# Optimization experiments

Hardware: AMD Instinct MI355X
Metric: run time of the kernel (lower is better)

## Reference

```python
import jax, jax.numpy as jnp
import numpy as np

B, C, H, W = 128, 8, 144, 144
TW, OG = 5, 2          # token_window, off_grid
NCLS, DT = 6, 256      # num_cls, dim_token
ITC = C * H * TW       # in_token_channel = 5760
EPS = 1e-5


def setup_inputs() -> dict:
    key = jax.random.key(0)
    ks = jax.random.split(key, 40)
    n = jax.random.normal
    u = jax.random.uniform
    CW = C * W  # 1152
    inp = {
        'x': n(ks[0], (B, C, H, W), jnp.float32),
        # ext head: Conv1d(1152,256,1) -> BN(256) -> Conv1d(256,2,1)
        'ext_w1': n(ks[1], (256, CW)) * 0.02, 'ext_b1': jnp.zeros((256,)),
        'ext_g': jnp.ones((256,)), 'ext_bb': jnp.zeros((256,)),
        'ext_m': n(ks[2], (256,)) * 0.1, 'ext_v': u(ks[3], (256,), minval=0.5, maxval=1.5),
        'ext_w2': n(ks[4], (2, 256)) * 0.05, 'ext_b2': jnp.zeros((2,)),
        # cls head: Conv1d(1152,256,1) -> BN(256) -> Conv1d(256,144,1)
        'cls_w1': n(ks[5], (256, CW)) * 0.02, 'cls_b1': jnp.zeros((256,)),
        'cls_g': jnp.ones((256,)), 'cls_bb': jnp.zeros((256,)),
        'cls_m': n(ks[6], (256,)) * 0.1, 'cls_v': u(ks[7], (256,), minval=0.5, maxval=1.5),
        'cls_w2': n(ks[8], (W, 256)) * 0.05, 'cls_b2': jnp.zeros((W,)),
        # to_token Linear(5760,256) and class embeddings
        'tok_w': n(ks[9], (ITC, DT)) * 0.01, 'tok_b': jnp.zeros((DT,)),
        'emb': n(ks[10], (NCLS, DT)),
        # transformer (depth=1, heads=2, dim_head=32 -> inner=64)
        'ln1_g': jnp.ones((DT,)), 'ln1_b': jnp.zeros((DT,)),
        'qkv_w': n(ks[11], (DT, 3 * 64)) * 0.05,
        'out_w': n(ks[12], (64, DT)) * 0.05, 'out_b': jnp.zeros((DT,)),
        'ln2_g': jnp.ones((DT,)), 'ln2_b': jnp.zeros((DT,)),
        'ff_w1': n(ks[13], (DT, 512)) * 0.05, 'ff_b1': jnp.zeros((512,)),
        'ff_w2': n(ks[14], (512, DT)) * 0.05, 'ff_b2': jnp.zeros((DT,)),
        'lnf_g': jnp.ones((DT,)), 'lnf_b': jnp.zeros((DT,)),
        'fin_w': n(ks[15], (DT, ITC)) * 0.02, 'fin_b': jnp.zeros((ITC,)),
    }
    return inp


def _ln(z, g, b):
    mu = jnp.mean(z, -1, keepdims=True)
    var = jnp.var(z, -1, keepdims=True)
    return (z - mu) * jax.lax.rsqrt(var + EPS) * g + b


def reference(x, ext_w1, ext_b1, ext_g, ext_bb, ext_m, ext_v, ext_w2, ext_b2,
              cls_w1, cls_b1, cls_g, cls_bb, cls_m, cls_v, cls_w2, cls_b2,
              tok_w, tok_b, emb,
              ln1_g, ln1_b, qkv_w, out_w, out_b,
              ln2_g, ln2_b, ff_w1, ff_b1, ff_w2, ff_b2,
              lnf_g, lnf_b, fin_w, fin_b):

    def head(row, w1, b1, g, bet, m, v, w2, b2):
        # row: [B, C*W, H]; 1x1 conv = per-position GEMM, BN in eval mode
        h = jnp.einsum('oc,bch->boh', w1, row) + b1[:, None]
        h = (h - m[:, None]) * jax.lax.rsqrt(v[:, None] + EPS) * g[:, None] + bet[:, None]
        h = jnp.einsum('oc,bch->boh', w2, h) + b2[:, None]
        return jnp.transpose(h, (0, 2, 1))  # [B, H, out]

    def heads_on(xx):
        # 'b c h w -> b (c w) h' (c major, w minor)
        row = jnp.transpose(xx, (0, 1, 3, 2)).reshape(B, C * W, H)
        e = jax.nn.softmax(head(row, ext_w1, ext_b1, ext_g, ext_bb, ext_m, ext_v, ext_w2, ext_b2), axis=2)
        c = jax.nn.softmax(head(row, cls_w1, cls_b1, cls_g, cls_bb, cls_m, cls_v, cls_w2, cls_b2), axis=2)
        return e, c

    ext, cls = heads_on(x)
    xp = jnp.pad(x, ((0, 0), (0, 0), (0, 0), (OG, OG)))  # [B,C,H,W+4]

    argmax_col = jnp.argmax(cls, axis=2)                  # [B,H]
    idx = argmax_col[:, :, None] + jnp.arange(TW)         # window in padded coords

    def transformer(t):  # t: [B, N, DT]
        z = _ln(t, ln1_g, ln1_b)
        q, k, v = jnp.split(z @ qkv_w, 3, axis=-1)
        sp = lambda a: a.reshape(B, -1, 2, 32).transpose(0, 2, 1, 3)  # b h n d
        q, k, v = sp(q), sp(k), sp(v)
        att = jax.nn.softmax(jnp.einsum('bhnd,bhmd->bhnm', q, k) * (32 ** -0.5), axis=-1)
        o = jnp.einsum('bhnm,bhmd->bhnd', att, v).transpose(0, 2, 1, 3).reshape(B, -1, 64)
        t = o @ out_w + out_b + t
        z = _ln(t, ln2_g, ln2_b)
        t = jax.nn.gelu(z @ ff_w1 + ff_b1, approximate=False) @ ff_w2 + ff_b2 + t
        t = _ln(t, lnf_g, lnf_b)
        return (t @ fin_w + fin_b).reshape(B, -1, C, H, TW)  # [B,N,C,H,TW]

    def refine(xpad):
        g_idx = jnp.broadcast_to(idx[:, None], (B, C, H, TW))
        patches = jnp.take_along_axis(xpad, g_idx, axis=3)    # [B,C,H,TW]
        tok = patches.reshape(B, -1) @ tok_w + tok_b          # [B,DT]
        tokens = tok[:, None, :] + emb[None]                  # [B,NCLS,DT]
        refined = transformer(tokens)                         # [B,NCLS,C,H,TW]
        xpt = jnp.transpose(xpad, (0, 2, 3, 1))               # [B,H,Wp,C]
        bb = jnp.arange(B)[:, None, None]
        hh = jnp.arange(H)[None, :, None]
        for i in range(NCLS):
            xpt = xpt.at[bb, hh, idx].set(jnp.transpose(refined[:, i], (0, 2, 3, 1)))
        return jnp.transpose(xpt, (0, 3, 1, 2))

    xp = jax.lax.cond(jnp.mean(ext[:, :, 0]) > 0.3, refine, lambda a: a, xp)
    x2 = xp[:, :, :, OG:W + OG]
    ext2, cls2 = heads_on(x2)
    return ext, cls, ext2, cls2
```

## Files before the change

kernel.cpp:

```cpp
#include <hip/hip_runtime.h>
#include <math.h>

#define EPSF 1e-5f
#define GAPTH 1e-3f
#define NKS 4
#define KSL 288
#define RROWS 18432


typedef __attribute__((ext_vector_type(8))) short short8v;
typedef __attribute__((ext_vector_type(4))) float f32x4;
typedef unsigned short ushort;
typedef unsigned int uint;

__device__ inline ushort f2bf(float f) {
    uint u = __float_as_uint(f);
    uint r = (u + 0x7FFFu + ((u >> 16) & 1u)) >> 16;
    return (ushort)r;
}
__device__ inline float bf2f(ushort h) { return __uint_as_float(((uint)h) << 16); }

__global__ __launch_bounds__(256) void wcomb_build(
    const float* __restrict__ w1e, const float* __restrict__ b1e, const float* __restrict__ ge,
    const float* __restrict__ bbe, const float* __restrict__ me, const float* __restrict__ ve,
    const float* __restrict__ w2e, const float* __restrict__ b2e,
    const float* __restrict__ w1c, const float* __restrict__ b1c, const float* __restrict__ gc,
    const float* __restrict__ bbc, const float* __restrict__ mc, const float* __restrict__ vc,
    const float* __restrict__ w2c, const float* __restrict__ b2c,
    float* __restrict__ Wc32, ushort* __restrict__ Wchi, ushort* __restrict__ Wclo,
    float* __restrict__ cconst)
{
    __shared__ float coef[256];
    __shared__ float csum[4];
    const int j = blockIdx.x, kq = blockIdx.y, tid = threadIdx.x;
    const int lane = tid & 63, wid = tid >> 6;

    const float *w1 = nullptr, *w2row = nullptr, *b1 = nullptr, *g = nullptr,
                *bb = nullptr, *m = nullptr, *v = nullptr;
    float b2v = 0.f;
    int valid = 0;
    if (j < 144) {
        valid = 1; w1 = w1c; w2row = w2c + (size_t)j * 256;
        b1 = b1c; g = gc; bb = bbc; m = mc; v = vc; b2v = b2c[j];
    } else if (j < 146) {
        valid = 1; w1 = w1e; w2row = w2e + (size_t)(j - 144) * 256;
        b1 = b1e; g = ge; bb = bbe; m = me; v = ve; b2v = b2e[j - 144];
    }

    float cf = 0.f, cc = 0.f;
    if (valid) {
        float s = g[tid] * rsqrtf(v[tid] + EPSF);
        float w2v = w2row[tid];
        cf = w2v * s;
        cc = w2v * ((b1[tid] - m[tid]) * s + bb[tid]);
    }
    coef[tid] = cf;
    if (kq == 0) {
        float t = cc;
#pragma unroll
        for (int off = 32; off; off >>= 1) t += __shfl_xor(t, off);
        if (lane == 0) csum[wid] = t;
    }
    __syncthreads();
    if (kq == 0 && tid == 0)
        cconst[j] = valid ? ((csum[0] + csum[1]) + (csum[2] + csum[3]) + b2v) : 0.f;

    for (int k = kq * KSL + tid; k < (kq + 1) * KSL; k += 256) {
        float acc = 0.f;
        if (valid) {
            for (int o = 0; o < 256; o++) acc += coef[o] * w1[(size_t)o * 1152 + k];
        }
        Wc32[(size_t)j * 1152 + k] = acc;
        ushort hi = f2bf(acc);
        Wchi[(size_t)j * 1152 + k] = hi;
        Wclo[(size_t)j * 1152 + k] = f2bf(acc - bf2f(hi));
    }
}

__global__ void zero_counters(int* __restrict__ cand_count)
{
    *cand_count = 0;
}

__global__ __launch_bounds__(256) void transpose_w(
    const float* __restrict__ src, float* __restrict__ dst, int R, int Cc)
{
    __shared__ float tile[32][33];
    const int rb = blockIdx.y * 32, cb = blockIdx.x * 32;
    const int tx = threadIdx.x & 31, ty = threadIdx.x >> 5;
#pragma unroll
    for (int i = ty; i < 32; i += 8) {
        int r = rb + i, c = cb + tx;
        tile[i][tx] = (r < R && c < Cc) ? src[(size_t)r * Cc + c] : 0.f;
    }
    __syncthreads();
#pragma unroll
    for (int i = ty; i < 32; i += 8) {
        int c = cb + i, r = rb + tx;
        if (c < Cc && r < R) dst[(size_t)c * R + r] = tile[tx][i];
    }
}

__global__ __launch_bounds__(256) void logits_gemm(
    const float* __restrict__ x, const ushort* __restrict__ Wchi, const ushort* __restrict__ Wclo,
    float* __restrict__ logits_part)
{
    __shared__ ushort Ahi[128][40], Alo[128][40], Bhi[160][40], Blo[160][40];
    const int tid = threadIdx.x;
    const int lane = tid & 63, wid = tid >> 6;
    const int wm = wid & 1, wn = wid >> 1;
    const int rb = blockIdx.x * 128;
    const int ks = blockIdx.y;
    const int kbase = ks * KSL;
    const int NIT = KSL / 32;

    const int rl = tid >> 1, kq = (tid & 1) << 4;
    const int arow = rb + rl;
    const int ab = arow / 144, ahh = arow - ab * 144;
    const int br2 = 128 + (tid >> 1);

    float av[16];
    short8v vb0a, vb0b, vl0a, vl0b;
    short8v vb2a, vb2b, vl2a, vl2b;

    auto LOAD = [&](int kb) {
        const int k0 = kb + kq;
        const int c = k0 / 144, w = k0 - c * 144;
        const float* xp = x + (((size_t)(ab * 8 + c) * 144 + ahh) * 144 + w);
#pragma unroll
        for (int q = 0; q < 4; q++) {
            const float4 t4 = *reinterpret_cast<const float4*>(xp + q * 4);
            av[q * 4 + 0] = t4.x; av[q * 4 + 1] = t4.y;
            av[q * 4 + 2] = t4.z; av[q * 4 + 3] = t4.w;
        }
        const ushort* bh = Wchi + (size_t)rl * 1152 + k0;
        const ushort* bl = Wclo + (size_t)rl * 1152 + k0;
        vb0a = *reinterpret_cast<const short8v*>(bh);
        vb0b = *reinterpret_cast<const short8v*>(bh + 8);
        vl0a = *reinterpret_cast<const short8v*>(bl);
        vl0b = *reinterpret_cast<const short8v*>(bl + 8);
        if (tid < 64) {
            const ushort* bh2 = Wchi + (size_t)br2 * 1152 + k0;
            const ushort* bl2 = Wclo + (size_t)br2 * 1152 + k0;
            vb2a = *reinterpret_cast<const short8v*>(bh2);
            vb2b = *reinterpret_cast<const short8v*>(bh2 + 8);
            vl2a = *reinterpret_cast<const short8v*>(bl2);
            vl2b = *reinterpret_cast<const short8v*>(bl2 + 8);
        }
    };

    auto STORE = [&]() {
        short8v hv0, hv1, lv0, lv1;
#pragma unroll
        for (int q = 0; q < 8; q++) {
            ushort h = f2bf(av[q]);
            hv0[q] = (short)h; lv0[q] = (short)f2bf(av[q] - bf2f(h));
        }
#pragma unroll
        for (int q = 0; q < 8; q++) {
            ushort h = f2bf(av[8 + q]);
            hv1[q] = (short)h; lv1[q] = (short)f2bf(av[8 + q] - bf2f(h));
        }
        *reinterpret_cast<short8v*>(&Ahi[rl][kq]) = hv0;
        *reinterpret_cast<short8v*>(&Ahi[rl][kq + 8]) = hv1;
        *reinterpret_cast<short8v*>(&Alo[rl][kq]) = lv0;
        *reinterpret_cast<short8v*>(&Alo[rl][kq + 8]) = lv1;
        *reinterpret_cast<short8v*>(&Bhi[rl][kq]) = vb0a;
        *reinterpret_cast<short8v*>(&Bhi[rl][kq + 8]) = vb0b;
        *reinterpret_cast<short8v*>(&Blo[rl][kq]) = vl0a;
        *reinterpret_cast<short8v*>(&Blo[rl][kq + 8]) = vl0b;
        if (tid < 64) {
            *reinterpret_cast<short8v*>(&Bhi[br2][kq]) = vb2a;
            *reinterpret_cast<short8v*>(&Bhi[br2][kq + 8]) = vb2b;
            *reinterpret_cast<short8v*>(&Blo[br2][kq]) = vl2a;
            *reinterpret_cast<short8v*>(&Blo[br2][kq + 8]) = vl2b;
        }
    };

    f32x4 acc[4][5];
#pragma unroll
    for (int mt = 0; mt < 4; mt++)
#pragma unroll
        for (int nt = 0; nt < 5; nt++) acc[mt][nt] = (f32x4){0.f, 0.f, 0.f, 0.f};

    const int fr = lane & 15, fg = (lane >> 4) << 3;

    LOAD(kbase);
    for (int t = 0; t < NIT; t++) {
        STORE();
        if (t < NIT - 1) LOAD(kbase + (t + 1) * 32);
        __syncthreads();
        short8v ah[4], al[4];
#pragma unroll
        for (int mt = 0; mt < 4; mt++) {
            ah[mt] = *reinterpret_cast<const short8v*>(&Ahi[wm * 64 + mt * 16 + fr][fg]);
            al[mt] = *reinterpret_cast<const short8v*>(&Alo[wm * 64 + mt * 16 + fr][fg]);
        }
#pragma unroll
        for (int nt = 0; nt < 5; nt++) {
            short8v bh = *reinterpret_cast<const short8v*>(&Bhi[wn * 80 + nt * 16 + fr][fg]);
            short8v bl = *reinterpret_cast<const short8v*>(&Blo[wn * 80 + nt * 16 + fr][fg]);
#pragma unroll
            for (int mt = 0; mt < 4; mt++) {
                acc[mt][nt] = __builtin_amdgcn_mfma_f32_16x16x32_bf16(ah[mt], bh, acc[mt][nt], 0, 0, 0);
                acc[mt][nt] = __builtin_amdgcn_mfma_f32_16x16x32_bf16(ah[mt], bl, acc[mt][nt], 0, 0, 0);
                acc[mt][nt] = __builtin_amdgcn_mfma_f32_16x16x32_bf16(al[mt], bh, acc[mt][nt], 0, 0, 0);
            }
        }
        __syncthreads();
    }

    float* base = logits_part + (size_t)ks * RROWS * 160;
#pragma unroll
    for (int mt = 0; mt < 4; mt++) {
#pragma unroll
        for (int nt = 0; nt < 5; nt++) {
            int gcol = wn * 80 + nt * 16 + fr;
            if (gcol < 146) {
                float* dst = base + (size_t)(rb + wm * 64 + mt * 16 + ((lane >> 4) << 2)) * 160 + gcol;
#pragma unroll
                for (int i = 0; i < 4; i++)
                    dst[(size_t)i * 160] = acc[mt][nt][i];
            }
        }
    }
}

template<int DELTA>
__global__ __launch_bounds__(256) void softmax_heads(
    const float* __restrict__ logits_part, const float* __restrict__ cconst,
    float* __restrict__ out_cls, float* __restrict__ out_ext,
    int* __restrict__ amax, float* __restrict__ partials,
    int* __restrict__ cand_count, int* __restrict__ cand_list,
    const float* __restrict__ x, const float* __restrict__ WcT,
    const float* __restrict__ refined5, const int* __restrict__ flag)
{
    __shared__ float ps[4];
    __shared__ float dL[4][148];
    __shared__ float dsh[4][40];
    __shared__ int   ksh[4][40];
    const int r4 = threadIdx.x >> 6, lane = threadIdx.x & 63;
    const int row = blockIdx.x * 4 + r4;

    if (DELTA) {
        const int fl = *flag;
        if (fl) {
            const int b = row / 144, hh = row - b * 144;
            const int a = amax[row];
            if (lane < 40) {
                int c = lane / 5, tw = lane - c * 5;
                int w = a - 2 + tw;
                float d = 0.f; int k = 0;
                if (w >= 0 && w < 144) {
                    k = c * 144 + w;
                    d = refined5[(size_t)b * 5760 + (c * 144 + hh) * 5 + tw]
                      - x[((size_t)(b * 8 + c) * 144 + hh) * 144 + w];
                }
                dsh[r4][lane] = d; ksh[r4][lane] = k;
            }
            __syncthreads();
#pragma unroll
            for (int rj = 0; rj < 3; rj++) {
                int j = lane + rj * 64;
                if (j < 146) {
                    float acc = 0.f;
#pragma unroll 8
                    for (int i = 0; i < 40; i++)
                        acc += WcT[(size_t)ksh[r4][i] * 160 + j] * dsh[r4][i];
                    dL[r4][j] = acc;
                }
            }
        } else {
#pragma unroll
            for (int rj = 0; rj < 3; rj++) {
                int j = lane + rj * 64;
                if (j < 146) dL[r4][j] = 0.f;
            }
        }
        __syncthreads();
    }

    const float* L0 = logits_part + (size_t)row * 160;
    const float* L1 = L0 + (size_t)RROWS * 160;
    const float* L2 = L1 + (size_t)RROWS * 160;
    const float* L3 = L2 + (size_t)RROWS * 160;
    float v0 = L0[lane] + L1[lane] + L2[lane] + L3[lane] + cconst[lane];
    float v1 = L0[lane + 64] + L1[lane + 64] + L2[lane + 64] + L3[lane + 64] + cconst[lane + 64];
    float v2 = (lane < 16) ? (L0[lane + 128] + L1[lane + 128] + L2[lane + 128] + L3[lane + 128]
                              + cconst[lane + 128])
                           : -3.0e38f;
    if (DELTA) {
        v0 += dL[r4][lane];
        v1 += dL[r4][lane + 64];
        if (lane < 16) v2 += dL[r4][lane + 128];
    }
    float m = v0; int mi = lane;
    if (v1 > m) { m = v1; mi = lane + 64; }
    if (v2 > m) { m = v2; mi = lane + 128; }
    float m1 = v0, m2 = -3.0e38f;
    if (v1 > m1) { m2 = m1; m1 = v1; } else m2 = v1;
    if (v2 > m1) { m2 = m1; m1 = v2; } else m2 = fmaxf(m2, v2);
#pragma unroll
    for (int off = 32; off; off >>= 1) {
        float om = __shfl_xor(m, off);
        int   oi = __shfl_xor(mi, off);
        if (om > m || (om == m && oi < mi)) { m = om; mi = oi; }
        float om1 = __shfl_xor(m1, off);
        float om2 = __shfl_xor(m2, off);
        float nm1 = fmaxf(m1, om1);
        m2 = fmaxf(fminf(m1, om1), fmaxf(m2, om2));
        m1 = nm1;
    }
    float e0 = expf(v0 - m), e1 = expf(v1 - m);
    float e2 = (lane < 16) ? expf(v2 - m) : 0.f;
    float s = e0 + e1 + e2;
#pragma unroll
    for (int off = 32; off; off >>= 1) s += __shfl_xor(s, off);
    float inv = 1.f / s;
    float* O = out_cls + (size_t)row * 144;
    O[lane] = e0 * inv;
    O[lane + 64] = e1 * inv;
    if (lane < 16) O[lane + 128] = e2 * inv;

    float l0 = L0[144] + L1[144] + L2[144] + L3[144] + cconst[144];
    float l1 = L0[145] + L1[145] + L2[145] + L3[145] + cconst[145];
    if (DELTA) { l0 += dL[r4][144]; l1 += dL[r4][145]; }
    float mx = fmaxf(l0, l1);
    float ee0 = expf(l0 - mx), ee1 = expf(l1 - mx);
    float einv = 1.f / (ee0 + ee1);
    float p0 = ee0 * einv;
    if (lane == 0) {
        out_ext[(size_t)row * 2] = p0;
        out_ext[(size_t)row * 2 + 1] = ee1 * einv;
        if (amax != nullptr && !DELTA) {
            amax[row] = mi;
            if (m1 - m2 < GAPTH) {
                int slot = atomicAdd(cand_count, 1);
                cand_list[slot] = row;
            }
        }
    }
    if (partials != nullptr) {
        if (lane == 0) ps[r4] = p0;
        __syncthreads();
        if (threadIdx.x == 0) partials[blockIdx.x] = (ps[0] + ps[1]) + (ps[2] + ps[3]);
    }
}

__global__ __launch_bounds__(256) void reduce_flag(const float* __restrict__ partials, int n,
                                                   int* __restrict__ flag)
{
    __shared__ float sm[256];
    int tid = threadIdx.x;
    float s = 0.f;
    for (int i = tid; i < n; i += 256) s += partials[i];
    sm[tid] = s; __syncthreads();
    for (int off = 128; off; off >>= 1) {
        if (tid < off) sm[tid] += sm[tid + off];
        __syncthreads();
    }
    if (tid == 0) *flag = (sm[0] * (1.f / 18432.f) > 0.3f) ? 1 : 0;
}

__global__ __launch_bounds__(256) void fixup_list(
    const int* __restrict__ cand_count, const int* __restrict__ cand_list,
    const float* __restrict__ x,
    const float* __restrict__ w1cT, const float* __restrict__ b1c,
    const float* __restrict__ gc, const float* __restrict__ bbc,
    const float* __restrict__ mc, const float* __restrict__ vc,
    const float* __restrict__ w2cT, const float* __restrict__ b2c,
    int* __restrict__ amax)
{
    __shared__ float xrow[1152];
    __shared__ float hsh[256];
    __shared__ float Lsh[144];
    const int tid = threadIdx.x;
    const int n = *cand_count;

    for (int ci = blockIdx.x; ci < n; ci += gridDim.x) {
        const int row = cand_list[ci];
        const int b = row / 144, hh = row - b * 144;
        for (int e = tid; e < 1152; e += 256) {
            int c = e / 144, w = e - c * 144;
            xrow[e] = x[(((size_t)(b * 8 + c) * 144 + hh) * 144) + w];
        }
        __syncthreads();
        {
            float a = 0.f;
#pragma unroll 8
            for (int k = 0; k < 1152; k++) a += w1cT[(size_t)k * 256 + tid] * xrow[k];
            float sc = gc[tid] * rsqrtf(vc[tid] + EPSF);
            hsh[tid] = (a + b1c[tid] - mc[tid]) * sc + bbc[tid];
        }
        __syncthreads();
        if (tid < 144) {
            float a = 0.f;
#pragma unroll 8
            for (int k = 0; k < 256; k++) a += w2cT[(size_t)k * 144 + tid] * hsh[k];
            Lsh[tid] = a + b2c[tid];
        }
        __syncthreads();
        if (tid == 0) {
            int bi = 0; float bv = Lsh[0];
            for (int j = 1; j < 144; j++) if (Lsh[j] > bv) { bv = Lsh[j]; bi = j; }
            amax[row] = bi;
        }
        __syncthreads();
    }
}

__global__ __launch_bounds__(256) void tok_partial(const float* __restrict__ x,
    const int* __restrict__ amax, const float* __restrict__ tok_w, float* __restrict__ tpart)
{
    __shared__ float P[720];
    __shared__ int ash[144];
    int b = blockIdx.x, c = blockIdx.y, tid = threadIdx.x;
    if (tid < 144) ash[tid] = amax[b * 144 + tid];
    __syncthreads();
    for (int e = tid; e < 720; e += 256) {
        int hh = e / 5, tw = e - hh * 5;
        int w = ash[hh] + tw - 2;
        P[e] = (w >= 0 && w < 144) ? x[(((size_t)(b * 8 + c) * 144 + hh) * 144) + w] : 0.f;
    }
    __syncthreads();
    const float* wbase = tok_w + (size_t)c * 720 * 256;
    float a0 = 0.f, a1 = 0.f, a2 = 0.f, a3 = 0.f;
    for (int k = 0; k < 720; k += 4) {
        a0 += P[k]     * wbase[(size_t)k * 256 + tid];
        a1 += P[k + 1] * wbase[(size_t)(k + 1) * 256 + tid];
        a2 += P[k + 2] * wbase[(size_t)(k + 2) * 256 + tid];
        a3 += P[k + 3] * wbase[(size_t)(k + 3) * 256 + tid];
    }
    tpart[((size_t)b * 8 + c) * 256 + tid] = (a0 + a1) + (a2 + a3);
}

__global__ __launch_bounds__(512) void attn_front(
    const float* __restrict__ tpart, const float* __restrict__ tok_b,
    const float* __restrict__ emb,
    const float* __restrict__ ln1_g, const float* __restrict__ ln1_b,
    const float* __restrict__ qkv_w,
    const float* __restrict__ out_w, const float* __restrict__ out_b,
    const float* __restrict__ ln2_g, const float* __restrict__ ln2_b,
    float* __restrict__ z2_5, float* __restrict__ t5out)
{
    __shared__ float s[256];
    __shared__ float z[6][256];
    __shared__ float qk[6][192];
    __shared__ float att[2][6];
    __shared__ float o5[64];
    __shared__ float t5[256];
    __shared__ float stat[2];
    const int b = blockIdx.x, tid = threadIdx.x;
    const int lane = tid & 63, wv = tid >> 6;
    const int g4 = tid >> 2, l4 = tid & 3;

    if (tid < 256) {
        float a = tok_b[tid];
#pragma unroll
        for (int ks = 0; ks < 8; ks++) a += tpart[((size_t)b * 8 + ks) * 256 + tid];
        s[tid] = a;
    }
    __syncthreads();

    if (wv < 6) {
        float y[4], s1 = 0.f, s2 = 0.f;
#pragma unroll
        for (int q = 0; q < 4; q++) {
            int k = lane + 64 * q;
            y[q] = s[k] + emb[wv * 256 + k];
            s1 += y[q]; s2 += y[q] * y[q];
        }
#pragma unroll
        for (int off = 32; off; off >>= 1) { s1 += __shfl_xor(s1, off); s2 += __shfl_xor(s2, off); }
        float mu = s1 * (1.f / 256.f);
        float var = s2 * (1.f / 256.f) - mu * mu;
        float rs = rsqrtf(var + EPSF);
#pragma unroll
        for (int q = 0; q < 4; q++) {
            int k = lane + 64 * q;
            z[wv][k] = (y[q] - mu) * rs * ln1_g[k] + ln1_b[k];
        }
    }
    __syncthreads();

    for (int tt = g4; tt < 832; tt += 128) {
        int i, c;
        if (tt < 768) { i = tt >> 7; c = 64 + (tt & 127); }
        else          { i = 5;       c = tt - 768; }
        float a = 0.f;
#pragma unroll 8
        for (int j = 0; j < 64; j++) {
            int k = l4 + 4 * j;
            a += z[i][k] * qkv_w[(size_t)k * 192 + c];
        }
        a += __shfl_xor(a, 1);
        a += __shfl_xor(a, 2);
        if (l4 == 0) qk[i][c] = a;
    }
    __syncthreads();

    if (tid < 12) {
        int h = tid / 6, j = tid - h * 6;
        float a = 0.f;
#pragma unroll
        for (int d = 0; d < 32; d++) a += qk[5][h * 32 + d] * qk[j][64 + h * 32 + d];
        att[h][j] = a * 0.17677669529663687f;
    }
    __syncthreads();
    if (tid < 2) {
        float m = -3.0e38f;
        for (int j = 0; j < 6; j++) m = fmaxf(m, att[tid][j]);
        float ssum = 0.f;
        for (int j = 0; j < 6; j++) { float e = expf(att[tid][j] - m); att[tid][j] = e; ssum += e; }
        float inv = 1.f / ssum;
        for (int j = 0; j < 6; j++) att[tid][j] *= inv;
    }
    __syncthreads();
    if (tid < 64) {
        int h = tid >> 5;
        float a = 0.f;
#pragma unroll
        for (int j = 0; j < 6; j++) a += att[h][j] * qk[j][128 + tid];
        o5[tid] = a;
    }
    __syncthreads();

    for (int tt = g4; tt < 256; tt += 128) {
        float a = 0.f;
#pragma unroll
        for (int j = 0; j < 16; j++) {
            int d = l4 + 4 * j;
            a += o5[d] * out_w[(size_t)d * 256 + tt];
        }
        a += __shfl_xor(a, 1);
        a += __shfl_xor(a, 2);
        if (l4 == 0) t5[tt] = a + out_b[tt] + s[tt] + emb[5 * 256 + tt];
    }
    __syncthreads();

    if (wv == 0) {
        float s1 = 0.f, s2 = 0.f;
#pragma unroll
        for (int q = 0; q < 4; q++) { float vv = t5[lane + 64 * q]; s1 += vv; s2 += vv * vv; }
#pragma unroll
        for (int off = 32; off; off >>= 1) { s1 += __shfl_xor(s1, off); s2 += __shfl_xor(s2, off); }
        if (lane == 0) {
            float mu = s1 * (1.f / 256.f);
            float var = s2 * (1.f / 256.f) - mu * mu;
            stat[0] = mu; stat[1] = rsqrtf(var + EPSF);
        }
    }
    __syncthreads();
    if (tid < 256) {
        t5out[(size_t)b * 256 + tid] = t5[tid];
        z2_5[(size_t)b * 256 + tid] = (t5[tid] - stat[0]) * stat[1] * ln2_g[tid] + ln2_b[tid];
    }
}

__global__ __launch_bounds__(512) void ff1_gelu(
    const float* __restrict__ z2_5, const float* __restrict__ ff_w1,
    const float* __restrict__ ff_b1, float* __restrict__ f5)
{
    __shared__ float zsh[256];
    const int b = blockIdx.x, half = blockIdx.y, tid = threadIdx.x;
    const int g4 = tid >> 2, l4 = tid & 3;
    if (tid < 256) zsh[tid] = z2_5[(size_t)b * 256 + tid];
    __syncthreads();
    for (int tt = g4; tt < 256; tt += 128) {
        const int jj = half * 256 + tt;
        float a = 0.f;
#pragma unroll 8
        for (int j = 0; j < 64; j++) {
            int k = l4 + 4 * j;
            a += zsh[k] * ff_w1[(size_t)k * 512 + jj];
        }
        a += __shfl_xor(a, 1);
        a += __shfl_xor(a, 2);
        if (l4 == 0) {
            a += ff_b1[jj];
            f5[(size_t)b * 512 + jj] = 0.5f * a * (1.f + erff(a * 0.70710678118654752f));
        }
    }
}

__global__ __launch_bounds__(512) void ff2_lnf(
    const float* __restrict__ f5, const float* __restrict__ ff_w2,
    const float* __restrict__ ff_b2, const float* __restrict__ t5in,
    const float* __restrict__ lnf_g, const float* __restrict__ lnf_b,
    float* __restrict__ tfin)
{
    __shared__ float fsh[512];
    __shared__ float tsh[256];
    __shared__ float stat[2];
    const int b = blockIdx.x, tid = threadIdx.x;
    const int lane = tid & 63, wv = tid >> 6;
    const int g4 = tid >> 2, l4 = tid & 3;
    fsh[tid] = f5[(size_t)b * 512 + tid];
    __syncthreads();
    for (int tt = g4; tt < 256; tt += 128) {
        float a = 0.f;
#pragma unroll 8
        for (int j = 0; j < 128; j++) {
            int k = l4 + 4 * j;
            a += fsh[k] * ff_w2[(size_t)k * 256 + tt];
        }
        a += __shfl_xor(a, 1);
        a += __shfl_xor(a, 2);
        if (l4 == 0) tsh[tt] = a + ff_b2[tt] + t5in[(size_t)b * 256 + tt];
    }
    __syncthreads();
    if (wv == 0) {
        float s1 = 0.f, s2 = 0.f;
#pragma unroll
        for (int q = 0; q < 4; q++) { float vv = tsh[lane + 64 * q]; s1 += vv; s2 += vv * vv; }
#pragma unroll
        for (int off = 32; off; off >>= 1) { s1 += __shfl_xor(s1, off); s2 += __shfl_xor(s2, off); }
        if (lane == 0) {
            float mu = s1 * (1.f / 256.f);
            float var = s2 * (1.f / 256.f) - mu * mu;
            stat[0] = mu; stat[1] = rsqrtf(var + EPSF);
        }
    }
    __syncthreads();
    if (tid < 256)
        tfin[(size_t)b * 256 + tid] = (tsh[tid] - stat[0]) * stat[1] * lnf_g[tid] + lnf_b[tid];
}

__global__ __launch_bounds__(256) void fin_gemm(const float* __restrict__ tfin,
    const float* __restrict__ fin_w, const float* __restrict__ fin_b, float* __restrict__ refined5)
{
    __shared__ float tf[16][256];
    int tid = threadIdx.x;
    int nb = blockIdx.x * 256 + tid;
    int bg = blockIdx.y * 16;
    for (int e = tid; e < 4096; e += 256) tf[e >> 8][e & 255] = tfin[(size_t)(bg + (e >> 8)) * 256 + (e & 255)];
    __syncthreads();
    if (nb < 5760) {
        float acc[16];
#pragma unroll
        for (int bb = 0; bb < 16; bb++) acc[bb] = 0.f;
        for (int k = 0; k < 256; k++) {
            float wv = fin_w[(size_t)k * 5760 + nb];
#pragma unroll
            for (int bb = 0; bb < 16; bb++) acc[bb] += tf[bb][k] * wv;
        }
        float fb = fin_b[nb];
#pragma unroll
        for (int bb = 0; bb < 16; bb++)
            refined5[(size_t)(bg + bb) * 5760 + nb] = acc[bb] + fb;
    }
}

extern "C" void kernel_launch(void* const* d_in, const int* in_sizes, int n_in,
                              void* d_out, int out_size, void* d_ws, size_t ws_size,
                              hipStream_t stream)
{
    const float* x      = (const float*)d_in[0];
    const float* ext_w1 = (const float*)d_in[1];
    const float* ext_b1 = (const float*)d_in[2];
    const float* ext_g  = (const float*)d_in[3];
    const float* ext_bb = (const float*)d_in[4];
    const float* ext_m  = (const float*)d_in[5];
    const float* ext_v  = (const float*)d_in[6];
    const float* ext_w2 = (const float*)d_in[7];
    const float* ext_b2 = (const float*)d_in[8];
    const float* cls_w1 = (const float*)d_in[9];
    const float* cls_b1 = (const float*)d_in[10];
    const float* cls_g  = (const float*)d_in[11];
    const float* cls_bb = (const float*)d_in[12];
    const float* cls_m  = (const float*)d_in[13];
    const float* cls_v  = (const float*)d_in[14];
    const float* cls_w2 = (const float*)d_in[15];
    const float* cls_b2 = (const float*)d_in[16];
    const float* tok_w  = (const float*)d_in[17];
    const float* tok_b  = (const float*)d_in[18];
    const float* emb    = (const float*)d_in[19];
    const float* ln1_g  = (const float*)d_in[20];
    const float* ln1_b  = (const float*)d_in[21];
    const float* qkv_w  = (const float*)d_in[22];
    const float* out_w  = (const float*)d_in[23];
    const float* out_b  = (const float*)d_in[24];
    const float* ln2_g  = (const float*)d_in[25];
    const float* ln2_b  = (const float*)d_in[26];
    const float* ff_w1  = (const float*)d_in[27];
    const float* ff_b1  = (const float*)d_in[28];
    const float* ff_w2  = (const float*)d_in[29];
    const float* ff_b2  = (const float*)d_in[30];
    const float* lnf_g  = (const float*)d_in[31];
    const float* lnf_b  = (const float*)d_in[32];
    const float* fin_w  = (const float*)d_in[33];
    const float* fin_b  = (const float*)d_in[34];

    float* out = (float*)d_out;
    float* ws  = (float*)d_ws;

    float*  Wc32     = ws;
    float*  cconst   = ws + 184320;
    ushort* Wchi     = (ushort*)(ws + 184480);
    ushort* Wclo     = (ushort*)(ws + 276640);
    float*  logitsP  = ws + 368800;
    float*  partials = ws + 12165280;
    float*  z2_5     = ws + 12169888;
    float*  t5buf    = ws + 12202656;
    float*  f5buf    = ws + 12235424;
    float*  tfin     = ws + 12300960;
    float*  refined5 = ws + 12333728;
    float*  tpart    = ws + 13071008;
    int*    amax     = (int*)(ws + 13333152);
    int*    flag     = (int*)(ws + 13351584);
    int*    cand_cnt = (int*)(ws + 13351585);
    int*    cand_lst = (int*)(ws + 13351586);
    float*  w1cT     = ws + 13370020;
    float*  w2cT     = ws + 13664932;
    float*  WcT      = ws + 13701796;

    float* out_ext  = out;
    float* out_cls  = out + 36864;
    float* out_ext2 = out + 2691072;
    float* out_cls2 = out + 2727936;

    dim3 blk(256);

    wcomb_build<<<dim3(160, 4), blk, 0, stream>>>(
        ext_w1, ext_b1, ext_g, ext_bb, ext_m, ext_v, ext_w2, ext_b2,
        cls_w1, cls_b1, cls_g, cls_bb, cls_m, cls_v, cls_w2, cls_b2,
        Wc32, Wchi, Wclo, cconst);
    zero_counters<<<1, 1, 0, stream>>>(cand_cnt);
    transpose_w<<<dim3(36, 8), blk, 0, stream>>>(cls_w1, w1cT, 256, 1152);
    transpose_w<<<dim3(8, 5), blk, 0, stream>>>(cls_w2, w2cT, 144, 256);
    transpose_w<<<dim3(36, 5), blk, 0, stream>>>(Wc32, WcT, 160, 1152);

    logits_gemm<<<dim3(144, NKS), blk, 0, stream>>>(x, Wchi, Wclo, logitsP);
    softmax_heads<0><<<4608, blk, 0, stream>>>(logitsP, cconst, out_cls, out_ext, amax, partials,
        cand_cnt, cand_lst, nullptr, nullptr, nullptr, nullptr);
    reduce_flag<<<1, blk, 0, stream>>>(partials, 4608, flag);
    fixup_list<<<256, blk, 0, stream>>>(cand_cnt, cand_lst, x,
        w1cT, cls_b1, cls_g, cls_bb, cls_m, cls_v, w2cT, cls_b2, amax);

    tok_partial<<<dim3(128, 8), blk, 0, stream>>>(x, amax, tok_w, tpart);
    attn_front<<<128, dim3(512), 0, stream>>>(tpart, tok_b, emb, ln1_g, ln1_b, qkv_w,
        out_w, out_b, ln2_g, ln2_b, z2_5, t5buf);
    ff1_gelu<<<dim3(128, 2), dim3(512), 0, stream>>>(z2_5, ff_w1, ff_b1, f5buf);
    ff2_lnf<<<128, dim3(512), 0, stream>>>(f5buf, ff_w2, ff_b2, t5buf, lnf_g, lnf_b, tfin);
    fin_gemm<<<dim3(23, 8), blk, 0, stream>>>(tfin, fin_w, fin_b, refined5);

    softmax_heads<1><<<4608, blk, 0, stream>>>(logitsP, cconst, out_cls2, out_ext2, amax, nullptr,
        nullptr, nullptr, x, WcT, refined5, flag);
}
```

Measured before the change: 307.8 us.

## Halve logits GEMM M-tile, halve split-K, and lower ambiguity threshold

The logits GEMM now uses 64-row tiles with 2 K-splits instead of 128-row tiles with 4, so the grid doubles in M while the partial-logit buffer and the softmax reduction shrink from four partials to two. Workspace offsets are repacked to match. The fixup kernel's dot products are split into four independent accumulators to add ILP. GAPTH is lowered, so fewer rows count as argmax candidates needing exact fp32 recompute. That saves fixup work but relies on the bf16 hi/lo split GEMM being precise enough near ties.

New measurement: 278.3 us. 9.6% less time.

```diff
diff --git a/kernel.cpp b/kernel.cpp
--- a/kernel.cpp
+++ b/kernel.cpp
@@ -2,9 +2,9 @@
 #include <math.h>
 
 #define EPSF 1e-5f
-#define GAPTH 1e-3f
-#define NKS 4
-#define KSL 288
+#define GAPTH 2e-4f
+#define NKS 2
+#define KSL 576
 #define RROWS 18432
 
 
@@ -65,7 +65,7 @@
     if (kq == 0 && tid == 0)
         cconst[j] = valid ? ((csum[0] + csum[1]) + (csum[2] + csum[3]) + b2v) : 0.f;
 
-    for (int k = kq * KSL + tid; k < (kq + 1) * KSL; k += 256) {
+    for (int k = kq * 288 + tid; k < (kq + 1) * 288; k += 256) {
         float acc = 0.f;
         if (valid) {
             for (int o = 0; o < 256; o++) acc += coef[o] * w1[(size_t)o * 1152 + k];
@@ -105,81 +105,69 @@
     const float* __restrict__ x, const ushort* __restrict__ Wchi, const ushort* __restrict__ Wclo,
     float* __restrict__ logits_part)
 {
-    __shared__ ushort Ahi[128][40], Alo[128][40], Bhi[160][40], Blo[160][40];
+    __shared__ ushort Ahi[64][40], Alo[64][40], Bhi[160][40], Blo[160][40];
     const int tid = threadIdx.x;
     const int lane = tid & 63, wid = tid >> 6;
     const int wm = wid & 1, wn = wid >> 1;
-    const int rb = blockIdx.x * 128;
+    const int rb = blockIdx.x * 64;
     const int ks = blockIdx.y;
     const int kbase = ks * KSL;
     const int NIT = KSL / 32;
 
-    const int rl = tid >> 1, kq = (tid & 1) << 4;
+    const int rl = tid >> 2, kk = (tid & 3) << 3;
     const int arow = rb + rl;
     const int ab = arow / 144, ahh = arow - ab * 144;
-    const int br2 = 128 + (tid >> 1);
-
-    float av[16];
-    short8v vb0a, vb0b, vl0a, vl0b;
-    short8v vb2a, vb2b, vl2a, vl2b;
+
+    const int br0 = tid >> 2, bk0 = (tid & 3) << 3;
+    const int br2 = 128 + (tid >> 2), bk2 = (tid & 3) << 3;
+
+    float av[8];
+    short8v vbh0, vbl0, vbh1, vbl1, vbh2, vbl2;
 
     auto LOAD = [&](int kb) {
-        const int k0 = kb + kq;
-        const int c = k0 / 144, w = k0 - c * 144;
-        const float* xp = x + (((size_t)(ab * 8 + c) * 144 + ahh) * 144 + w);
-#pragma unroll
-        for (int q = 0; q < 4; q++) {
-            const float4 t4 = *reinterpret_cast<const float4*>(xp + q * 4);
-            av[q * 4 + 0] = t4.x; av[q * 4 + 1] = t4.y;
-            av[q * 4 + 2] = t4.z; av[q * 4 + 3] = t4.w;
-        }
-        const ushort* bh = Wchi + (size_t)rl * 1152 + k0;
-        const ushort* bl = Wclo + (size_t)rl * 1152 + k0;
-        vb0a = *reinterpret_cast<const short8v*>(bh);
-        vb0b = *reinterpret_cast<const short8v*>(bh + 8);
-        vl0a = *reinterpret_cast<const short8v*>(bl);
-        vl0b = *reinterpret_cast<const short8v*>(bl + 8);
-        if (tid < 64) {
-            const ushort* bh2 = Wchi + (size_t)br2 * 1152 + k0;
-            const ushort* bl2 = Wclo + (size_t)br2 * 1152 + k0;
-            vb2a = *reinterpret_cast<const short8v*>(bh2);
-            vb2b = *reinterpret_cast<const short8v*>(bh2 + 8);
-            vl2a = *reinterpret_cast<const short8v*>(bl2);
-            vl2b = *reinterpret_cast<const short8v*>(bl2 + 8);
+        int k1 = kb + kk, c1 = k1 / 144, w1 = k1 - c1 * 144;
+        const float4 t0 = *reinterpret_cast<const float4*>(
+            x + (((size_t)(ab * 8 + c1) * 144 + ahh) * 144 + w1));
+        const float4 t1 = *reinterpret_cast<const float4*>(
+            x + (((size_t)(ab * 8 + c1) * 144 + ahh) * 144 + w1 + 4));
+        av[0] = t0.x; av[1] = t0.y; av[2] = t0.z; av[3] = t0.w;
+        av[4] = t1.x; av[5] = t1.y; av[6] = t1.z; av[7] = t1.w;
+        size_t o0 = (size_t)br0 * 1152 + kb + bk0;
+        vbh0 = *reinterpret_cast<const short8v*>(Wchi + o0);
+        vbl0 = *reinterpret_cast<const short8v*>(Wclo + o0);
+        size_t o1 = (size_t)(br0 + 64) * 1152 + kb + bk0;
+        vbh1 = *reinterpret_cast<const short8v*>(Wchi + o1);
+        vbl1 = *reinterpret_cast<const short8v*>(Wclo + o1);
+        if (tid < 128) {
+            size_t o2 = (size_t)br2 * 1152 + kb + bk2;
+            vbh2 = *reinterpret_cast<const short8v*>(Wchi + o2);
+            vbl2 = *reinterpret_cast<const short8v*>(Wclo + o2);
         }
     };
 
     auto STORE = [&]() {
-        short8v hv0, hv1, lv0, lv1;
+        short8v hv, lv;
 #pragma unroll
         for (int q = 0; q < 8; q++) {
             ushort h = f2bf(av[q]);
-            hv0[q] = (short)h; lv0[q] = (short)f2bf(av[q] - bf2f(h));
-        }
-#pragma unroll
-        for (int q = 0; q < 8; q++) {
-            ushort h = f2bf(av[8 + q]);
-            hv1[q] = (short)h; lv1[q] = (short)f2bf(av[8 + q] - bf2f(h));
-        }
-        *reinterpret_cast<short8v*>(&Ahi[rl][kq]) = hv0;
-        *reinterpret_cast<short8v*>(&Ahi[rl][kq + 8]) = hv1;
-        *reinterpret_cast<short8v*>(&Alo[rl][kq]) = lv0;
-        *reinterpret_cast<short8v*>(&Alo[rl][kq + 8]) = lv1;
-        *reinterpret_cast<short8v*>(&Bhi[rl][kq]) = vb0a;
-        *reinterpret_cast<short8v*>(&Bhi[rl][kq + 8]) = vb0b;
-        *reinterpret_cast<short8v*>(&Blo[rl][kq]) = vl0a;
-        *reinterpret_cast<short8v*>(&Blo[rl][kq + 8]) = vl0b;
-        if (tid < 64) {
-            *reinterpret_cast<short8v*>(&Bhi[br2][kq]) = vb2a;
-            *reinterpret_cast<short8v*>(&Bhi[br2][kq + 8]) = vb2b;
-            *reinterpret_cast<short8v*>(&Blo[br2][kq]) = vl2a;
-            *reinterpret_cast<short8v*>(&Blo[br2][kq + 8]) = vl2b;
+            hv[q] = (short)h;
+            lv[q] = (short)f2bf(av[q] - bf2f(h));
+        }
+        *reinterpret_cast<short8v*>(&Ahi[rl][kk]) = hv;
+        *reinterpret_cast<short8v*>(&Alo[rl][kk]) = lv;
+        *reinterpret_cast<short8v*>(&Bhi[br0][bk0]) = vbh0;
+        *reinterpret_cast<short8v*>(&Blo[br0][bk0]) = vbl0;
+        *reinterpret_cast<short8v*>(&Bhi[br0 + 64][bk0]) = vbh1;
+        *reinterpret_cast<short8v*>(&Blo[br0 + 64][bk0]) = vbl1;
+        if (tid < 128) {
+            *reinterpret_cast<short8v*>(&Bhi[br2][bk2]) = vbh2;
+            *reinterpret_cast<short8v*>(&Blo[br2][bk2]) = vbl2;
         }
     };
 
-    f32x4 acc[4][5];
-#pragma unroll
-    for (int mt = 0; mt < 4; mt++)
+    f32x4 acc[2][5];
+#pragma unroll
+    for (int mt = 0; mt < 2; mt++)
 #pragma unroll
         for (int nt = 0; nt < 5; nt++) acc[mt][nt] = (f32x4){0.f, 0.f, 0.f, 0.f};
 
@@ -190,34 +178,32 @@
         STORE();
         if (t < NIT - 1) LOAD(kbase + (t + 1) * 32);
         __syncthreads();
-        short8v ah[4], al[4];
-#pragma unroll
-        for (int mt = 0; mt < 4; mt++) {
-            ah[mt] = *reinterpret_cast<const short8v*>(&Ahi[wm * 64 + mt * 16 + fr][fg]);
-            al[mt] = *reinterpret_cast<const short8v*>(&Alo[wm * 64 + mt * 16 + fr][fg]);
-        }
+        short8v ah0 = *reinterpret_cast<const short8v*>(&Ahi[wm * 32 + fr][fg]);
+        short8v al0 = *reinterpret_cast<const short8v*>(&Alo[wm * 32 + fr][fg]);
+        short8v ah1 = *reinterpret_cast<const short8v*>(&Ahi[wm * 32 + 16 + fr][fg]);
+        short8v al1 = *reinterpret_cast<const short8v*>(&Alo[wm * 32 + 16 + fr][fg]);
 #pragma unroll
         for (int nt = 0; nt < 5; nt++) {
             short8v bh = *reinterpret_cast<const short8v*>(&Bhi[wn * 80 + nt * 16 + fr][fg]);
             short8v bl = *reinterpret_cast<const short8v*>(&Blo[wn * 80 + nt * 16 + fr][fg]);
-#pragma unroll
-            for (int mt = 0; mt < 4; mt++) {
-                acc[mt][nt] = __builtin_amdgcn_mfma_f32_16x16x32_bf16(ah[mt], bh, acc[mt][nt], 0, 0, 0);
-                acc[mt][nt] = __builtin_amdgcn_mfma_f32_16x16x32_bf16(ah[mt], bl, acc[mt][nt], 0, 0, 0);
-                acc[mt][nt] = __builtin_amdgcn_mfma_f32_16x16x32_bf16(al[mt], bh, acc[mt][nt], 0, 0, 0);
-            }
+            acc[0][nt] = __builtin_amdgcn_mfma_f32_16x16x32_bf16(ah0, bh, acc[0][nt], 0, 0, 0);
+            acc[0][nt] = __builtin_amdgcn_mfma_f32_16x16x32_bf16(ah0, bl, acc[0][nt], 0, 0, 0);
+            acc[0][nt] = __builtin_amdgcn_mfma_f32_16x16x32_bf16(al0, bh, acc[0][nt], 0, 0, 0);
+            acc[1][nt] = __builtin_amdgcn_mfma_f32_16x16x32_bf16(ah1, bh, acc[1][nt], 0, 0, 0);
+            acc[1][nt] = __builtin_amdgcn_mfma_f32_16x16x32_bf16(ah1, bl, acc[1][nt], 0, 0, 0);
+            acc[1][nt] = __builtin_amdgcn_mfma_f32_16x16x32_bf16(al1, bh, acc[1][nt], 0, 0, 0);
         }
         __syncthreads();
     }
 
     float* base = logits_part + (size_t)ks * RROWS * 160;
 #pragma unroll
-    for (int mt = 0; mt < 4; mt++) {
+    for (int mt = 0; mt < 2; mt++) {
 #pragma unroll
         for (int nt = 0; nt < 5; nt++) {
             int gcol = wn * 80 + nt * 16 + fr;
             if (gcol < 146) {
-                float* dst = base + (size_t)(rb + wm * 64 + mt * 16 + ((lane >> 4) << 2)) * 160 + gcol;
+                float* dst = base + (size_t)(rb + wm * 32 + mt * 16 + ((lane >> 4) << 2)) * 160 + gcol;
 #pragma unroll
                 for (int i = 0; i < 4; i++)
                     dst[(size_t)i * 160] = acc[mt][nt][i];
@@ -282,12 +268,9 @@
 
     const float* L0 = logits_part + (size_t)row * 160;
     const float* L1 = L0 + (size_t)RROWS * 160;
-    const float* L2 = L1 + (size_t)RROWS * 160;
-    const float* L3 = L2 + (size_t)RROWS * 160;
-    float v0 = L0[lane] + L1[lane] + L2[lane] + L3[lane] + cconst[lane];
-    float v1 = L0[lane + 64] + L1[lane + 64] + L2[lane + 64] + L3[lane + 64] + cconst[lane + 64];
-    float v2 = (lane < 16) ? (L0[lane + 128] + L1[lane + 128] + L2[lane + 128] + L3[lane + 128]
-                              + cconst[lane + 128])
+    float v0 = L0[lane] + L1[lane] + cconst[lane];
+    float v1 = L0[lane + 64] + L1[lane + 64] + cconst[lane + 64];
+    float v2 = (lane < 16) ? (L0[lane + 128] + L1[lane + 128] + cconst[lane + 128])
                            : -3.0e38f;
     if (DELTA) {
         v0 += dL[r4][lane];
@@ -322,8 +305,8 @@
     O[lane + 64] = e1 * inv;
     if (lane < 16) O[lane + 128] = e2 * inv;
 
-    float l0 = L0[144] + L1[144] + L2[144] + L3[144] + cconst[144];
-    float l1 = L0[145] + L1[145] + L2[145] + L3[145] + cconst[145];
+    float l0 = L0[144] + L1[144] + cconst[144];
+    float l1 = L0[145] + L1[145] + cconst[145];
     if (DELTA) { l0 += dL[r4][144]; l1 += dL[r4][145]; }
     float mx = fmaxf(l0, l1);
     float ee0 = expf(l0 - mx), ee1 = expf(l1 - mx);
@@ -386,18 +369,29 @@
         }
         __syncthreads();
         {
-            float a = 0.f;
-#pragma unroll 8
-            for (int k = 0; k < 1152; k++) a += w1cT[(size_t)k * 256 + tid] * xrow[k];
+            float a0 = 0.f, a1 = 0.f, a2 = 0.f, a3 = 0.f;
+#pragma unroll 4
+            for (int k = 0; k < 1152; k += 4) {
+                a0 += w1cT[(size_t)k * 256 + tid] * xrow[k];
+                a1 += w1cT[(size_t)(k + 1) * 256 + tid] * xrow[k + 1];
+                a2 += w1cT[(size_t)(k + 2) * 256 + tid] * xrow[k + 2];
+                a3 += w1cT[(size_t)(k + 3) * 256 + tid] * xrow[k + 3];
+            }
+            float a = (a0 + a1) + (a2 + a3);
             float sc = gc[tid] * rsqrtf(vc[tid] + EPSF);
             hsh[tid] = (a + b1c[tid] - mc[tid]) * sc + bbc[tid];
         }
         __syncthreads();
         if (tid < 144) {
-            float a = 0.f;
-#pragma unroll 8
-            for (int k = 0; k < 256; k++) a += w2cT[(size_t)k * 144 + tid] * hsh[k];
-            Lsh[tid] = a + b2c[tid];
+            float a0 = 0.f, a1 = 0.f, a2 = 0.f, a3 = 0.f;
+#pragma unroll 4
+            for (int k = 0; k < 256; k += 4) {
+                a0 += w2cT[(size_t)k * 144 + tid] * hsh[k];
+                a1 += w2cT[(size_t)(k + 1) * 144 + tid] * hsh[k + 1];
+                a2 += w2cT[(size_t)(k + 2) * 144 + tid] * hsh[k + 2];
+                a3 += w2cT[(size_t)(k + 3) * 144 + tid] * hsh[k + 3];
+            }
+            Lsh[tid] = (a0 + a1) + (a2 + a3) + b2c[tid];
         }
         __syncthreads();
         if (tid == 0) {
@@ -699,20 +693,20 @@
     ushort* Wchi     = (ushort*)(ws + 184480);
     ushort* Wclo     = (ushort*)(ws + 276640);
     float*  logitsP  = ws + 368800;
-    float*  partials = ws + 12165280;
-    float*  z2_5     = ws + 12169888;
-    float*  t5buf    = ws + 12202656;
-    float*  f5buf    = ws + 12235424;
-    float*  tfin     = ws + 12300960;
-    float*  refined5 = ws + 12333728;
-    float*  tpart    = ws + 13071008;
-    int*    amax     = (int*)(ws + 13333152);
-    int*    flag     = (int*)(ws + 13351584);
-    int*    cand_cnt = (int*)(ws + 13351585);
-    int*    cand_lst = (int*)(ws + 13351586);
-    float*  w1cT     = ws + 13370020;
-    float*  w2cT     = ws + 13664932;
-    float*  WcT      = ws + 13701796;
+    float*  partials = ws + 6267040;
+    float*  z2_5     = ws + 6271648;
+    float*  t5buf    = ws + 6304416;
+    float*  f5buf    = ws + 6337184;
+    float*  tfin     = ws + 6402720;
+    float*  refined5 = ws + 6435488;
+    float*  tpart    = ws + 7172768;
+    int*    amax     = (int*)(ws + 7434912);
+    int*    flag     = (int*)(ws + 7453344);
+    int*    cand_cnt = (int*)(ws + 7453345);
+    int*    cand_lst = (int*)(ws + 7453346);
+    float*  w1cT     = ws + 7471780;
+    float*  w2cT     = ws + 7766692;
+    float*  WcT      = ws + 7803556;
 
     float* out_ext  = out;
     float* out_cls  = out + 36864;
@@ -730,7 +724,7 @@
     transpose_w<<<dim3(8, 5), blk, 0, stream>>>(cls_w2, w2cT, 144, 256);
     transpose_w<<<dim3(36, 5), blk, 0, stream>>>(Wc32, WcT, 160, 1152);
 
-    logits_gemm<<<dim3(144, NKS), blk, 0, stream>>>(x, Wchi, Wclo, logitsP);
+    logits_gemm<<<dim3(288, NKS), blk, 0, stream>>>(x, Wchi, Wclo, logitsP);
     softmax_heads<0><<<4608, blk, 0, stream>>>(logitsP, cconst, out_cls, out_ext, amax, partials,
         cand_cnt, cand_lst, nullptr, nullptr, nullptr, nullptr);
     reduce_flag<<<1, blk, 0, stream>>>(partials, 4608, flag);
```
